# Optimization experiments

Measured on AMD Instinct MI355X. Metric: run time of the kernel, lower is better.

## Reference

```python
import jax, jax.numpy as jnp
import numpy as np

NUM_SITES = 64
BOND_DIM = 64
PHYS_DIM = 2
BATCH = 8192
INIT_STD = 0.125  # 1/sqrt(bond_dim)
EPS_AMP = 1e-12
EPS_LOG = 1e-30


def setup_inputs() -> dict:
    key = jax.random.key(0)
    k_cfg, k_l, k_b, k_r = jax.random.split(key, 4)
    configurations = jax.random.randint(k_cfg, (BATCH, NUM_SITES), 0, PHYS_DIM, dtype=jnp.int32)
    left = jax.random.normal(k_l, (PHYS_DIM, BOND_DIM), dtype=jnp.float32) * INIT_STD
    bulk = jax.random.normal(k_b, (NUM_SITES - 2, BOND_DIM, PHYS_DIM, BOND_DIM), dtype=jnp.float32) * INIT_STD
    right = jax.random.normal(k_r, (BOND_DIM, PHYS_DIM), dtype=jnp.float32) * INIT_STD
    return {"configurations": configurations, "left": left, "bulk": bulk, "right": right}


def _psi(configurations, left, bulk, right):
    # configurations: [B, S] int; left: [d, D]; bulk: [S-2, D, d, D]; right: [D, d]
    B = configurations.shape[0]
    env0 = left[configurations[:, 0]]  # [B, D]
    cfg_mid = configurations[:, 1:-1].T  # [S-2, B]

    def step(env, xs):
        site_t, idx = xs  # site_t: [D, d, D], idx: [B]
        D = site_t.shape[0]
        # env @ site (contract left bond), then gather the per-sample physical slice
        tmp = (env @ site_t.reshape(D, -1)).reshape(B, PHYS_DIM, D)  # [B, d, D]
        env = jnp.take_along_axis(tmp, idx[:, None, None], axis=1)[:, 0, :]  # [B, D]
        return env, None

    env, _ = jax.lax.scan(step, env0, (bulk, cfg_mid))
    cols = jnp.take(right, configurations[:, -1], axis=1).T  # [B, D]
    return jnp.sum(env * cols, axis=1)  # [B]


def _log_norm(left, bulk, right):
    env0 = left.T @ left  # [D, D]  (real dtype -> conj trivial)

    def step(carry, site_t):
        env, log_scale = carry
        sm = jnp.transpose(site_t, (1, 0, 2))  # [d, D, D]
        env = jnp.einsum('pdi,de,pej->ij', sm, env, sm)  # sum_p A_p^H env A_p
        scale = jnp.maximum(jnp.max(jnp.abs(env)), EPS_LOG)
        return (env / scale, log_scale + jnp.log(scale)), None

    (env, log_scale), _ = jax.lax.scan(step, (env0, jnp.zeros((), left.dtype)), bulk)
    z = jnp.sum(right * (env @ right))
    return jnp.log(jnp.maximum(z, EPS_LOG)) + log_scale


def reference(configurations, left, bulk, right):
    psi = _psi(configurations, left, bulk, right)
    abs_sq = jnp.maximum(psi * psi, EPS_AMP)
    log_z = _log_norm(left, bulk, right)
    nll = -(jnp.log(abs_sq) - log_z)
    return jnp.mean(nll)
```

## Files before the change

kernel.cpp:

```cpp
#include <hip/hip_runtime.h>
#include <math.h>

#define NBULK 62

typedef __attribute__((ext_vector_type(8))) short bf8_t;
typedef __attribute__((ext_vector_type(4))) float f4_t;

#define MFMA16(a, b, c) __builtin_amdgcn_mfma_f32_16x16x32_bf16((a), (b), (c), 0, 0, 0)

__device__ __forceinline__ unsigned short f2bf(float f) {
    unsigned int u = __float_as_uint(f);
    return (unsigned short)((u + 0x7FFFu + ((u >> 16) & 1u)) >> 16);
}
__device__ __forceinline__ float bf2f(unsigned short h) {
    return __uint_as_float(((unsigned int)h) << 16);
}
__device__ __forceinline__ unsigned cvtpk(float lo, float hi) {
    unsigned r;
    asm("v_cvt_pk_bf16_f32 %0, %1, %2" : "=v"(r) : "v"(lo), "v"(hi));
    return r;
}

__device__ __forceinline__ void gload16(const void* g, void* l) {
    __builtin_amdgcn_global_load_lds(
        (const __attribute__((address_space(1))) unsigned int*)g,
        (__attribute__((address_space(3))) unsigned int*)l, 16, 0, 0);
}

#define WS_E_OFF   1024
#define WS_B_OFF   6144
#define WS_NFF_OFF 45056
#define WS_NFB_OFF 1060864


extern "C" __global__ __launch_bounds__(256)
void mps_precompute(const float* __restrict__ bulkG,
                    unsigned short* __restrict__ NFfG,
                    unsigned short* __restrict__ NFbG,
                    float* __restrict__ wsF)
{
    __shared__ unsigned short Ff[8192];
    __shared__ unsigned short Fb[8192];
    const int s = blockIdx.x, tid = threadIdx.x;
    if (s == 0 && tid == 0) {
        wsF[0] = 0.f; wsF[1] = 0.f; wsF[2] = 0.f; wsF[3] = 0.f;
    }
    const float4* src = (const float4*)(bulkG + (size_t)s * 8192);
    for (int c = 0; c < 8; ++c) {
        int idx = tid + c * 256;
        float4 v = src[idx];
        int f  = idx * 4;
        int kk = f >> 7;
        int p  = (f >> 6) & 1;
        int j0 = f & 63;
        float vals[4] = {v.x, v.y, v.z, v.w};
        int qf = (kk >> 2) & 3, rf = kk & 3, mf = kk >> 4;
        int ksf = mf >> 1, jjf = (mf & 1) * 4 + rf;
        int tb = kk >> 4, lnb = kk & 15;
        #pragma unroll
        for (int t2 = 0; t2 < 4; ++t2) {
            int j = j0 + t2;
            unsigned short b = f2bf(vals[t2]);
            int tf = j >> 4, lnf = j & 15;
            Ff[((p * 4 + tf) * 2 + ksf) * 512 + (qf * 16 + lnf) * 8 + jjf] = b;
            int qb = (j >> 2) & 3, rb = j & 3, mb = j >> 4;
            int ksb = mb >> 1, jjb = (mb & 1) * 4 + rb;
            Fb[((p * 4 + tb) * 2 + ksb) * 512 + (qb * 16 + lnb) * 8 + jjb] = b;
        }
    }
    __syncthreads();
    const uint4* ff4 = (const uint4*)Ff;
    const uint4* fb4 = (const uint4*)Fb;
    uint4* fg = (uint4*)(NFfG + (size_t)s * 8192);
    uint4* bg = (uint4*)(NFbG + (size_t)s * 8192);
    for (int c = 0; c < 4; ++c) {
        int idx = tid + c * 256;
        fg[idx] = ff4[idx];
        bg[idx] = fb4[idx];
    }
}

__device__ __forceinline__ void pfetch(uint4 (&F)[16], const char* tb, int l16)
{
    #pragma unroll
    for (int i = 0; i < 16; ++i)
        F[i] = *(const uint4*)(tb + i * 1024 + l16);
}

__device__ __forceinline__ void pstep(f4_t (&a)[2][4], const uint4 (&F)[16],
                                      const bf8_t (&B)[2])
{
    #pragma unroll
    for (int p = 0; p < 2; ++p)
        #pragma unroll
        for (int mt = 0; mt < 4; ++mt) { f4_t z = {0.f, 0.f, 0.f, 0.f}; a[p][mt] = z; }
    #pragma unroll
    for (int ks = 0; ks < 2; ++ks)
        #pragma unroll
        for (int p = 0; p < 2; ++p)
            #pragma unroll
            for (int mt = 0; mt < 4; ++mt)
                a[p][mt] = MFMA16(*(const bf8_t*)&F[(p * 4 + mt) * 2 + ks], B[ks], a[p][mt]);
}

__device__ __forceinline__ void ppack(bf8_t (&B)[2], const f4_t (&a)[2][4], bool takeB)
{
    #pragma unroll
    for (int ks = 0; ks < 2; ++ks) {
        unsigned w[4];
        #pragma unroll
        for (int d = 0; d < 4; ++d) {
            int mt = 2 * ks + (d >> 1), r = (d & 1) * 2;
            float x0 = takeB ? a[1][mt][r]     : a[0][mt][r];
            float x1 = takeB ? a[1][mt][r + 1] : a[0][mt][r + 1];
            w[d] = cvtpk(x0, x1);
        }
        uint4 u = {w[0], w[1], w[2], w[3]};
        B[ks] = *(const bf8_t*)&u;
    }
}

extern "C" __global__ __launch_bounds__(256, 1)
void mps_main(const int* __restrict__ cfgG, const float* __restrict__ leftG,
              const float* __restrict__ rightG, float* __restrict__ wsF,
              const unsigned short* __restrict__ NFfG,
              const unsigned short* __restrict__ NFbG)
{
    extern __shared__ char smem[];
    const int tid  = threadIdx.x;
    const int bid  = blockIdx.x;
    const int wv   = tid >> 6;
    const int lane = tid & 63;
    const int ln   = lane & 15, q = lane >> 4;
    const int l16  = lane * 16;

    if (bid >= 2) {
        const char* NF = (const char*)NFfG;
        uint4 Fa[16], Fb[16];
        pfetch(Fa, NF, l16);
        pfetch(Fb, NF + 16384, l16);
        const int s0 = (bid - 2) * 64 + wv * 16;
        unsigned part = 0;
        {
            const int4* crow = (const int4*)(cfgG + (size_t)(s0 + ln) * 64 + q * 16);
            #pragma unroll
            for (int c = 0; c < 4; ++c) {
                int4 v = crow[c];
                part |= (unsigned)(v.x & 1) << (c * 4 + 0);
                part |= (unsigned)(v.y & 1) << (c * 4 + 1);
                part |= (unsigned)(v.z & 1) << (c * 4 + 2);
                part |= (unsigned)(v.w & 1) << (c * 4 + 3);
            }
        }
        unsigned pp   = __shfl_xor(part, 16);
        unsigned comb = (q & 1) ? (pp | (part << 16)) : (part | (pp << 16));
        unsigned selLo = __shfl(comb, ln);
        unsigned selHi = __shfl(comb, ln + 32);

        bf8_t B[2];
        {
            const float* lp = leftG + (selLo & 1u) * 64;
            #pragma unroll
            for (int ks = 0; ks < 2; ++ks) {
                unsigned w[4];
                #pragma unroll
                for (int d = 0; d < 4; ++d) {
                    int k0 = 16 * (2 * ks + (d >> 1)) + 4 * q + 2 * (d & 1);
                    w[d] = (unsigned)f2bf(lp[k0]) | ((unsigned)f2bf(lp[k0 + 1]) << 16);
                }
                uint4 u = {w[0], w[1], w[2], w[3]};
                B[ks] = *(const bf8_t*)&u;
            }
        }
        f4_t a[2][4];
        #define SELBIT(i) ((bool)((((i) < 32) ? (selLo >> (i)) : (selHi >> ((i) - 32))) & 1u))
        for (int t = 0; t < 60; t += 2) {
            pstep(a, Fa, B);
            pfetch(Fa, NF + (size_t)(t + 2) * 16384, l16);
            __builtin_amdgcn_sched_barrier(0);
            ppack(B, a, SELBIT(t + 1));
            pstep(a, Fb, B);
            pfetch(Fb, NF + (size_t)(t + 3) * 16384, l16);
            __builtin_amdgcn_sched_barrier(0);
            ppack(B, a, SELBIT(t + 2));
        }
        pstep(a, Fa, B);
        ppack(B, a, SELBIT(61));
        pstep(a, Fb, B);
        {
            bool tb2 = SELBIT(62);
            int selL = (int)(selHi >> 31) & 1;
            float psum = 0.f;
            #pragma unroll
            for (int mt = 0; mt < 4; ++mt)
                #pragma unroll
                for (int r = 0; r < 4; ++r) {
                    float v = tb2 ? a[1][mt][r] : a[0][mt][r];
                    psum = fmaf(v, rightG[(16 * mt + 4 * q + r) * 2 + selL], psum);
                }
            psum += __shfl_xor(psum, 16);
            psum += __shfl_xor(psum, 32);
            float lp2 = (lane < 16) ? logf(fmaxf(psum * psum, 1e-12f)) : 0.f;
            #pragma unroll
            for (int o = 1; o < 64; o <<= 1) lp2 += __shfl_xor(lp2, o);
            if (lane == 0) atomicAdd(&wsF[0], lp2);
        }
        #undef SELBIT
    } else {
        unsigned short* Ms0 = (unsigned short*)smem;
        unsigned short* Ms1 = Ms0 + 8192;
        unsigned short* XsS = Ms1 + 8192;
        float* wredS = (float*)(XsS + 8192);

        const bool fwd = (bid == 0);
        const char* NF = fwd ? (const char*)NFfG : (const char*)NFbG;
        {
            const char* g = NF + (size_t)(fwd ? 0 : 61) * 16384;
            for (int c = 0; c < 4; ++c) {
                int chunk = wv * 4 + c;
                gload16(g + chunk * 1024 + (size_t)lane * 16, (char*)Ms0 + chunk * 1024);
            }
        }
        bf8_t A1[4][2];
        {
            float li0[4], li1[4];
            #pragma unroll
            for (int mt = 0; mt < 4; ++mt) {
                int m = mt * 16 + ln;
                li0[mt] = fwd ? leftG[m]      : rightG[m * 2];
                li1[mt] = fwd ? leftG[64 + m] : rightG[m * 2 + 1];
            }
            #pragma unroll
            for (int ks = 0; ks < 2; ++ks) {
                float k0v[8], k1v[8];
                #pragma unroll
                for (int jj = 0; jj < 8; ++jj) {
                    int K = 16 * (2 * ks + (jj >> 2)) + 4 * q + (jj & 3);
                    k0v[jj] = fwd ? leftG[K]      : rightG[K * 2];
                    k1v[jj] = fwd ? leftG[64 + K] : rightG[K * 2 + 1];
                }
                #pragma unroll
                for (int mt = 0; mt < 4; ++mt) {
                    unsigned w[4];
                    #pragma unroll
                    for (int d = 0; d < 4; ++d) {
                        float x0 = li0[mt] * k0v[2 * d]     + li1[mt] * k1v[2 * d];
                        float x1 = li0[mt] * k0v[2 * d + 1] + li1[mt] * k1v[2 * d + 1];
                        w[d] = cvtpk(x0, x1);
                    }
                    uint4 u = {w[0], w[1], w[2], w[3]};
                    A1[mt][ks] = *(const bf8_t*)&u;
                }
            }
        }
        float lsum = 0.f;
        f4_t acc2s[2][4];
        for (int k = 0; k < 31; ++k) {
            __syncthreads();
            if (k > 0) {
                #pragma unroll
                for (int mt = 0; mt < 4; ++mt)
                    #pragma unroll
                    for (int ks = 0; ks < 2; ++ks)
                        A1[mt][ks] = *(const bf8_t*)&XsS[((k & 1) * 8 + mt * 2 + ks) * 512
                                                         + lane * 8];
            }
            const unsigned short* Msrc = (k & 1) ? Ms1 : Ms0;
            uint4 F[16];
            #pragma unroll
            for (int i = 0; i < 16; ++i)
                F[i] = *(const uint4*)(Msrc + i * 512 + lane * 8);
            bf8_t B1f[2][2];
            #pragma unroll
            for (int p = 0; p < 2; ++p)
                #pragma unroll
                for (int ks = 0; ks < 2; ++ks)
                    B1f[p][ks] = *(const bf8_t*)(Msrc + ((p * 4 + wv) * 2 + ks) * 512
                                                 + lane * 8);
            if (k + 1 < 31) {
                int sn = fwd ? (k + 1) : (61 - (k + 1));
                const char* g = NF + (size_t)sn * 16384;
                char* l = (char*)((k & 1) ? Ms0 : Ms1);
                for (int c = 0; c < 4; ++c) {
                    int chunk = wv * 4 + c;
                    gload16(g + chunk * 1024 + (size_t)lane * 16, l + chunk * 1024);
                }
            }
            float inv = 1.f;
            if (k > 0) {
                const float* wp = wredS + ((k - 1) & 1) * 4;
                float mm = fmaxf(fmaxf(wp[0], wp[1]), fmaxf(wp[2], wp[3]));
                float sc = fmaxf(mm, 1e-30f);
                inv = 1.f / sc;
                lsum += logf(sc);
            }
            #pragma unroll
            for (int p = 0; p < 2; ++p)
                #pragma unroll
                for (int mt = 0; mt < 4; ++mt) {
                    f4_t z = {0.f, 0.f, 0.f, 0.f};
                    acc2s[p][mt] = z;
                }
            #pragma unroll
            for (int p = 0; p < 2; ++p) {
                f4_t acc1[4];
                #pragma unroll
                for (int mt = 0; mt < 4; ++mt) { f4_t z = {0.f, 0.f, 0.f, 0.f}; acc1[mt] = z; }
                #pragma unroll
                for (int ks = 0; ks < 2; ++ks)
                    #pragma unroll
                    for (int mt = 0; mt < 4; ++mt)
                        acc1[mt] = MFMA16(A1[mt][ks], B1f[p][ks], acc1[mt]);
                bf8_t B2[2];
                #pragma unroll
                for (int ks = 0; ks < 2; ++ks) {
                    unsigned w[4];
                    #pragma unroll
                    for (int d = 0; d < 4; ++d) {
                        int mt = 2 * ks + (d >> 1), r = (d & 1) * 2;
                        w[d] = cvtpk(acc1[mt][r], acc1[mt][r + 1]);
                    }
                    uint4 u = {w[0], w[1], w[2], w[3]};
                    B2[ks] = *(const bf8_t*)&u;
                }
                #pragma unroll
                for (int ks = 0; ks < 2; ++ks)
                    #pragma unroll
                    for (int mt = 0; mt < 4; ++mt)
                        acc2s[p][mt] = MFMA16(*(const bf8_t*)&F[(p * 4 + mt) * 2 + ks],
                                              B2[ks], acc2s[p][mt]);
            }
            float mx = 0.f;
            #pragma unroll
            for (int mt = 0; mt < 4; ++mt)
                #pragma unroll
                for (int r = 0; r < 4; ++r) {
                    float x = (acc2s[0][mt][r] + acc2s[1][mt][r]) * inv;
                    acc2s[0][mt][r] = x;
                    mx = fmaxf(mx, fabsf(x));
                }
            #pragma unroll
            for (int ks = 0; ks < 2; ++ks) {
                unsigned w[4];
                #pragma unroll
                for (int d = 0; d < 4; ++d) {
                    int mt = 2 * ks + (d >> 1), r = (d & 1) * 2;
                    w[d] = cvtpk(acc2s[0][mt][r], acc2s[0][mt][r + 1]);
                }
                uint4 u = {w[0], w[1], w[2], w[3]};
                *(uint4*)&XsS[(((k + 1) & 1) * 8 + wv * 2 + ks) * 512 + lane * 8] = u;
            }
            #pragma unroll
            for (int o = 32; o > 0; o >>= 1) mx = fmaxf(mx, __shfl_xor(mx, o));
            if (lane == 0) wredS[(k & 1) * 4 + wv] = mx;
        }
        float* dst = wsF + (fwd ? WS_E_OFF : WS_B_OFF);
        #pragma unroll
        for (int mt = 0; mt < 4; ++mt)
            #pragma unroll
            for (int r = 0; r < 4; ++r)
                dst[(16 * mt + 4 * q + r) * 64 + wv * 16 + ln] = acc2s[0][mt][r];
        if (tid == 0) wsF[fwd ? 1 : 2] = lsum;
    }
}

extern "C" __global__ void mps_finalize(const float* __restrict__ wsF, float* __restrict__ out)
{
    const int lane = threadIdx.x;
    const float* E  = wsF + WS_E_OFF;
    const float* Bm = wsF + WS_B_OFF;
    float a = 0.f;
    #pragma unroll 8
    for (int j = 0; j < 64; ++j)
        a = fmaf(E[j * 64 + lane], Bm[j * 64 + lane], a);
    #pragma unroll
    for (int off = 32; off > 0; off >>= 1)
        a += __shfl_down(a, off);
    if (lane == 0) {
        const float z = fmaxf(a, 1e-30f);
        const float log_z = logf(z) + wsF[1] + wsF[2];
        out[0] = log_z - wsF[0] * (1.0f / 8192.0f);
    }
}

extern "C" void kernel_launch(void* const* d_in, const int* in_sizes, int n_in,
                              void* d_out, int out_size, void* d_ws, size_t ws_size,
                              hipStream_t stream)
{
    const int*   cfg   = (const int*)d_in[0];
    const float* left  = (const float*)d_in[1];
    const float* bulk  = (const float*)d_in[2];
    const float* right = (const float*)d_in[3];
    float* wsF = (float*)d_ws;
    unsigned short* NFf = (unsigned short*)((char*)d_ws + WS_NFF_OFF);
    unsigned short* NFb = (unsigned short*)((char*)d_ws + WS_NFB_OFF);

    mps_precompute<<<dim3(62), dim3(256), 0, stream>>>(bulk, NFf, NFb, wsF);
    mps_main<<<dim3(130), dim3(256), 49216, stream>>>(cfg, left, right, wsF, NFf, NFb);
    mps_finalize<<<dim3(1), dim3(64), 0, stream>>>(wsF, (float*)d_out);
}
```

Baseline: 104.8 us.

## Precompute paired-site transfer products to halve serial norm-chain steps

The precompute kernel gains 30 extra blocks that multiply adjacent bulk sites pairwise into combined 4-channel transfer tensors, stored in MFMA-ready bf16 layout. The serial log-norm chain in blocks 0/1 then runs 16 iterations instead of 31, each handling four physical-pair channels, with the last step using a single-site tensor. Operands are read directly from global memory instead of being staged through LDS with async loads. This shortens the serial critical path at the cost of extra precompute work and an extra bf16 rounding of pair products, which may reduce accuracy.

```diff
diff --git a/kernel.cpp b/kernel.cpp
--- a/kernel.cpp
+++ b/kernel.cpp
@@ -21,62 +21,130 @@
     return r;
 }
 
-__device__ __forceinline__ void gload16(const void* g, void* l) {
-    __builtin_amdgcn_global_load_lds(
-        (const __attribute__((address_space(1))) unsigned int*)g,
-        (__attribute__((address_space(3))) unsigned int*)l, 16, 0, 0);
-}
-
 #define WS_E_OFF   1024
 #define WS_B_OFF   6144
 #define WS_NFF_OFF 45056
 #define WS_NFB_OFF 1060864
+#define WS_PFF_OFF 2097152
+#define WS_PFB_OFF 2621440
 
 
 extern "C" __global__ __launch_bounds__(256)
 void mps_precompute(const float* __restrict__ bulkG,
                     unsigned short* __restrict__ NFfG,
                     unsigned short* __restrict__ NFbG,
+                    unsigned short* __restrict__ PFfG,
+                    unsigned short* __restrict__ PFbG,
                     float* __restrict__ wsF)
 {
-    __shared__ unsigned short Ff[8192];
-    __shared__ unsigned short Fb[8192];
+    extern __shared__ char smemP[];
     const int s = blockIdx.x, tid = threadIdx.x;
-    if (s == 0 && tid == 0) {
-        wsF[0] = 0.f; wsF[1] = 0.f; wsF[2] = 0.f; wsF[3] = 0.f;
-    }
-    const float4* src = (const float4*)(bulkG + (size_t)s * 8192);
-    for (int c = 0; c < 8; ++c) {
-        int idx = tid + c * 256;
-        float4 v = src[idx];
-        int f  = idx * 4;
-        int kk = f >> 7;
-        int p  = (f >> 6) & 1;
-        int j0 = f & 63;
-        float vals[4] = {v.x, v.y, v.z, v.w};
-        int qf = (kk >> 2) & 3, rf = kk & 3, mf = kk >> 4;
-        int ksf = mf >> 1, jjf = (mf & 1) * 4 + rf;
-        int tb = kk >> 4, lnb = kk & 15;
-        #pragma unroll
-        for (int t2 = 0; t2 < 4; ++t2) {
-            int j = j0 + t2;
-            unsigned short b = f2bf(vals[t2]);
-            int tf = j >> 4, lnf = j & 15;
-            Ff[((p * 4 + tf) * 2 + ksf) * 512 + (qf * 16 + lnf) * 8 + jjf] = b;
-            int qb = (j >> 2) & 3, rb = j & 3, mb = j >> 4;
-            int ksb = mb >> 1, jjb = (mb & 1) * 4 + rb;
-            Fb[((p * 4 + tb) * 2 + ksb) * 512 + (qb * 16 + lnb) * 8 + jjb] = b;
-        }
-    }
-    __syncthreads();
-    const uint4* ff4 = (const uint4*)Ff;
-    const uint4* fb4 = (const uint4*)Fb;
-    uint4* fg = (uint4*)(NFfG + (size_t)s * 8192);
-    uint4* bg = (uint4*)(NFbG + (size_t)s * 8192);
-    for (int c = 0; c < 4; ++c) {
-        int idx = tid + c * 256;
-        fg[idx] = ff4[idx];
-        bg[idx] = fb4[idx];
+    if (s < 62) {
+        unsigned short* Ff = (unsigned short*)smemP;
+        unsigned short* Fb = Ff + 8192;
+        if (s == 0 && tid == 0) {
+            wsF[0] = 0.f; wsF[1] = 0.f; wsF[2] = 0.f; wsF[3] = 0.f;
+        }
+        const float4* src = (const float4*)(bulkG + (size_t)s * 8192);
+        for (int c = 0; c < 8; ++c) {
+            int idx = tid + c * 256;
+            float4 v = src[idx];
+            int f  = idx * 4;
+            int kk = f >> 7;
+            int p  = (f >> 6) & 1;
+            int j0 = f & 63;
+            float vals[4] = {v.x, v.y, v.z, v.w};
+            int qf = (kk >> 2) & 3, rf = kk & 3, mf = kk >> 4;
+            int ksf = mf >> 1, jjf = (mf & 1) * 4 + rf;
+            int tb = kk >> 4, lnb = kk & 15;
+            #pragma unroll
+            for (int t2 = 0; t2 < 4; ++t2) {
+                int j = j0 + t2;
+                unsigned short b = f2bf(vals[t2]);
+                int tf = j >> 4, lnf = j & 15;
+                Ff[((p * 4 + tf) * 2 + ksf) * 512 + (qf * 16 + lnf) * 8 + jjf] = b;
+                int qb = (j >> 2) & 3, rb = j & 3, mb = j >> 4;
+                int ksb = mb >> 1, jjb = (mb & 1) * 4 + rb;
+                Fb[((p * 4 + tb) * 2 + ksb) * 512 + (qb * 16 + lnb) * 8 + jjb] = b;
+            }
+        }
+        __syncthreads();
+        const uint4* ff4 = (const uint4*)Ff;
+        const uint4* fb4 = (const uint4*)Fb;
+        uint4* fg = (uint4*)(NFfG + (size_t)s * 8192);
+        uint4* bg = (uint4*)(NFbG + (size_t)s * 8192);
+        for (int c = 0; c < 4; ++c) {
+            int idx = tid + c * 256;
+            fg[idx] = ff4[idx];
+            bg[idx] = fb4[idx];
+        }
+    } else {
+        int pb = s - 62;
+        bool pf = pb < 15;
+        int u  = pf ? pb : pb - 15;
+        int sA = pf ? 2 * u     : 60 - 2 * u;
+        int sB = pf ? 2 * u + 1 : 61 - 2 * u;
+        unsigned short* A16 = (unsigned short*)smemP;
+        unsigned short* B16 = A16 + 8192;
+        unsigned short* Sc  = (unsigned short*)smemP;
+        {
+            const float4* sa4 = (const float4*)(bulkG + (size_t)sA * 8192);
+            const float4* sb4 = (const float4*)(bulkG + (size_t)sB * 8192);
+            for (int c = 0; c < 8; ++c) {
+                int i = tid + c * 256;
+                float4 va = sa4[i], vb = sb4[i];
+                A16[i * 4 + 0] = f2bf(va.x); A16[i * 4 + 1] = f2bf(va.y);
+                A16[i * 4 + 2] = f2bf(va.z); A16[i * 4 + 3] = f2bf(va.w);
+                B16[i * 4 + 0] = f2bf(vb.x); B16[i * 4 + 1] = f2bf(vb.y);
+                B16[i * 4 + 2] = f2bf(vb.z); B16[i * 4 + 3] = f2bf(vb.w);
+            }
+        }
+        __syncthreads();
+        const int d = tid >> 2, iBase = (tid & 3) * 16;
+        float acc[4][16];
+        #pragma unroll
+        for (int c = 0; c < 4; ++c)
+            #pragma unroll
+            for (int ii = 0; ii < 16; ++ii) acc[c][ii] = 0.f;
+        for (int e = 0; e < 64; ++e) {
+            float a0 = bf2f(A16[d * 128 + e]);
+            float a1 = bf2f(A16[d * 128 + 64 + e]);
+            const unsigned short* b0p = B16 + e * 128 + iBase;
+            const unsigned short* b1p = b0p + 64;
+            #pragma unroll
+            for (int ii = 0; ii < 16; ++ii) {
+                float b0 = bf2f(b0p[ii]), b1 = bf2f(b1p[ii]);
+                acc[0][ii] = fmaf(a0, b0, acc[0][ii]);
+                acc[1][ii] = fmaf(a0, b1, acc[1][ii]);
+                acc[2][ii] = fmaf(a1, b0, acc[2][ii]);
+                acc[3][ii] = fmaf(a1, b1, acc[3][ii]);
+            }
+        }
+        __syncthreads();
+        #pragma unroll
+        for (int c = 0; c < 4; ++c)
+            #pragma unroll
+            for (int ii = 0; ii < 16; ++ii) {
+                int i = iBase + ii;
+                unsigned short vbf = f2bf(acc[c][ii]);
+                int idx;
+                if (pf)
+                    idx = c * 4096 + ((i >> 4) * 2 + (d >> 5)) * 512
+                        + ((((d >> 2) & 3) * 16 + (i & 15)) << 3)
+                        + ((d >> 4) & 1) * 4 + (d & 3);
+                else
+                    idx = c * 4096 + ((d >> 4) * 2 + (i >> 5)) * 512
+                        + ((((i >> 2) & 3) * 16 + (d & 15)) << 3)
+                        + ((i >> 4) & 1) * 4 + (i & 3);
+                Sc[idx] = vbf;
+            }
+        __syncthreads();
+        uint4* dst = (uint4*)((pf ? (char*)PFfG : (char*)PFbG) + (size_t)u * 32768);
+        const uint4* src4 = (const uint4*)Sc;
+        for (int c = 0; c < 8; ++c) {
+            int i = tid + c * 256;
+            dst[i] = src4[i];
+        }
     }
 }
 
@@ -124,7 +192,9 @@
 void mps_main(const int* __restrict__ cfgG, const float* __restrict__ leftG,
               const float* __restrict__ rightG, float* __restrict__ wsF,
               const unsigned short* __restrict__ NFfG,
-              const unsigned short* __restrict__ NFbG)
+              const unsigned short* __restrict__ NFbG,
+              const unsigned short* __restrict__ PFfG,
+              const unsigned short* __restrict__ PFbG)
 {
     extern __shared__ char smem[];
     const int tid  = threadIdx.x;
@@ -207,20 +277,13 @@
         }
         #undef SELBIT
     } else {
-        unsigned short* Ms0 = (unsigned short*)smem;
-        unsigned short* Ms1 = Ms0 + 8192;
-        unsigned short* XsS = Ms1 + 8192;
+        unsigned short* XsS = (unsigned short*)smem;
         float* wredS = (float*)(XsS + 8192);
 
         const bool fwd = (bid == 0);
-        const char* NF = fwd ? (const char*)NFfG : (const char*)NFbG;
-        {
-            const char* g = NF + (size_t)(fwd ? 0 : 61) * 16384;
-            for (int c = 0; c < 4; ++c) {
-                int chunk = wv * 4 + c;
-                gload16(g + chunk * 1024 + (size_t)lane * 16, (char*)Ms0 + chunk * 1024);
-            }
-        }
+        const char* PF  = fwd ? (const char*)PFfG : (const char*)PFbG;
+        const char* SNG = fwd ? ((const char*)NFfG + (size_t)30 * 16384)
+                              : ((const char*)NFbG + (size_t)31 * 16384);
         bf8_t A1[4][2];
         {
             float li0[4], li1[4];
@@ -255,40 +318,21 @@
         }
         float lsum = 0.f;
         f4_t acc2s[2][4];
-        for (int k = 0; k < 31; ++k) {
+        for (int it = 0; it < 16; ++it) {
             __syncthreads();
-            if (k > 0) {
+            if (it > 0) {
                 #pragma unroll
                 for (int mt = 0; mt < 4; ++mt)
                     #pragma unroll
                     for (int ks = 0; ks < 2; ++ks)
-                        A1[mt][ks] = *(const bf8_t*)&XsS[((k & 1) * 8 + mt * 2 + ks) * 512
+                        A1[mt][ks] = *(const bf8_t*)&XsS[((it & 1) * 8 + mt * 2 + ks) * 512
                                                          + lane * 8];
             }
-            const unsigned short* Msrc = (k & 1) ? Ms1 : Ms0;
-            uint4 F[16];
-            #pragma unroll
-            for (int i = 0; i < 16; ++i)
-                F[i] = *(const uint4*)(Msrc + i * 512 + lane * 8);
-            bf8_t B1f[2][2];
-            #pragma unroll
-            for (int p = 0; p < 2; ++p)
-                #pragma unroll
-                for (int ks = 0; ks < 2; ++ks)
-                    B1f[p][ks] = *(const bf8_t*)(Msrc + ((p * 4 + wv) * 2 + ks) * 512
-                                                 + lane * 8);
-            if (k + 1 < 31) {
-                int sn = fwd ? (k + 1) : (61 - (k + 1));
-                const char* g = NF + (size_t)sn * 16384;
-                char* l = (char*)((k & 1) ? Ms0 : Ms1);
-                for (int c = 0; c < 4; ++c) {
-                    int chunk = wv * 4 + c;
-                    gload16(g + chunk * 1024 + (size_t)lane * 16, l + chunk * 1024);
-                }
-            }
+            const char* base = (it < 15) ? (PF + (size_t)it * 32768) : SNG;
+            const int nb = (it < 15) ? 4 : 2;
             float inv = 1.f;
-            if (k > 0) {
-                const float* wp = wredS + ((k - 1) & 1) * 4;
+            if (it > 0) {
+                const float* wp = wredS + ((it - 1) & 1) * 4;
                 float mm = fmaxf(fmaxf(wp[0], wp[1]), fmaxf(wp[2], wp[3]));
                 float sc = fmaxf(mm, 1e-30f);
                 inv = 1.f / sc;
@@ -302,7 +346,18 @@
                     acc2s[p][mt] = z;
                 }
             #pragma unroll
-            for (int p = 0; p < 2; ++p) {
+            for (int c = 0; c < 4; ++c) {
+                if (c >= nb) continue;
+                const char* br = base + c * 8192;
+                bf8_t B1c[2], A2c[4][2];
+                #pragma unroll
+                for (int ks = 0; ks < 2; ++ks)
+                    B1c[ks] = *(const bf8_t*)(br + (wv * 2 + ks) * 1024 + l16);
+                #pragma unroll
+                for (int mt = 0; mt < 4; ++mt)
+                    #pragma unroll
+                    for (int ks = 0; ks < 2; ++ks)
+                        A2c[mt][ks] = *(const bf8_t*)(br + (mt * 2 + ks) * 1024 + l16);
                 f4_t acc1[4];
                 #pragma unroll
                 for (int mt = 0; mt < 4; ++mt) { f4_t z = {0.f, 0.f, 0.f, 0.f}; acc1[mt] = z; }
@@ -310,7 +365,7 @@
                 for (int ks = 0; ks < 2; ++ks)
                     #pragma unroll
                     for (int mt = 0; mt < 4; ++mt)
-                        acc1[mt] = MFMA16(A1[mt][ks], B1f[p][ks], acc1[mt]);
+                        acc1[mt] = MFMA16(A1[mt][ks], B1c[ks], acc1[mt]);
                 bf8_t B2[2];
                 #pragma unroll
                 for (int ks = 0; ks < 2; ++ks) {
@@ -327,8 +382,7 @@
                 for (int ks = 0; ks < 2; ++ks)
                     #pragma unroll
                     for (int mt = 0; mt < 4; ++mt)
-                        acc2s[p][mt] = MFMA16(*(const bf8_t*)&F[(p * 4 + mt) * 2 + ks],
-                                              B2[ks], acc2s[p][mt]);
+                        acc2s[c & 1][mt] = MFMA16(A2c[mt][ks], B2[ks], acc2s[c & 1][mt]);
             }
             float mx = 0.f;
             #pragma unroll
@@ -348,11 +402,11 @@
                     w[d] = cvtpk(acc2s[0][mt][r], acc2s[0][mt][r + 1]);
                 }
                 uint4 u = {w[0], w[1], w[2], w[3]};
-                *(uint4*)&XsS[(((k + 1) & 1) * 8 + wv * 2 + ks) * 512 + lane * 8] = u;
+                *(uint4*)&XsS[(((it + 1) & 1) * 8 + wv * 2 + ks) * 512 + lane * 8] = u;
             }
             #pragma unroll
             for (int o = 32; o > 0; o >>= 1) mx = fmaxf(mx, __shfl_xor(mx, o));
-            if (lane == 0) wredS[(k & 1) * 4 + wv] = mx;
+            if (lane == 0) wredS[(it & 1) * 4 + wv] = mx;
         }
         float* dst = wsF + (fwd ? WS_E_OFF : WS_B_OFF);
         #pragma unroll
@@ -394,8 +448,11 @@
     float* wsF = (float*)d_ws;
     unsigned short* NFf = (unsigned short*)((char*)d_ws + WS_NFF_OFF);
     unsigned short* NFb = (unsigned short*)((char*)d_ws + WS_NFB_OFF);
-
-    mps_precompute<<<dim3(62), dim3(256), 0, stream>>>(bulk, NFf, NFb, wsF);
-    mps_main<<<dim3(130), dim3(256), 49216, stream>>>(cfg, left, right, wsF, NFf, NFb);
+    unsigned short* PFf = (unsigned short*)((char*)d_ws + WS_PFF_OFF);
+    unsigned short* PFb = (unsigned short*)((char*)d_ws + WS_PFB_OFF);
+
+    mps_precompute<<<dim3(92), dim3(256), 32768, stream>>>(bulk, NFf, NFb, PFf, PFb, wsF);
+    mps_main<<<dim3(130), dim3(256), 16416, stream>>>(cfg, left, right, wsF,
+                                                      NFf, NFb, PFf, PFb);
     mps_finalize<<<dim3(1), dim3(64), 0, stream>>>(wsF, (float*)d_out);
 }
```

New measurement: 118.4 us. 1.13x slower.
